# Kernel tuning notes

Hardware: AMD Instinct MI355X
Metric: run time of the kernel (lower is better)

Reference implementation:

```python
import jax, jax.numpy as jnp
import numpy as np

FEATURE_DIM = 512
HIDDEN_DIM = 512
N_HEADS = 8
HEAD_DIM = HIDDEN_DIM // N_HEADS
MAX_LEN = 5000
GAMMA = 0.5  # gaussian relative-position bias width
LN_EPS = 1e-5


def make_pe(d_model, max_len):
    # sinusoidal positional encoding buffer, as in PositionalEncoding.__init__
    pos = jnp.arange(max_len, dtype=jnp.float32)[:, None]
    div = jnp.exp(jnp.arange(0, d_model, 2, dtype=jnp.float32) * (-np.log(10000.0) / d_model))
    ang = pos * div  # [max_len, d_model/2]
    pe = jnp.zeros((max_len, d_model), dtype=jnp.float32)
    pe = pe.at[:, 0::2].set(jnp.sin(ang)).at[:, 1::2].set(jnp.cos(ang))
    return pe


def setup_inputs() -> dict:
    key = jax.random.key(0)
    k_x, k_q, k_k, k_v = jax.random.split(key, 4)
    xavier = np.sqrt(6.0 / (FEATURE_DIM + HEAD_DIM))  # xavier_uniform over last two dims
    return {
        "data_window": jax.random.normal(k_x, (1, 2048, FEATURE_DIM), dtype=jnp.float32),
        "W_query": jax.random.uniform(k_q, (N_HEADS, FEATURE_DIM, HEAD_DIM), jnp.float32, -xavier, xavier),
        "W_key": jax.random.uniform(k_k, (N_HEADS, FEATURE_DIM, HEAD_DIM), jnp.float32, -xavier, xavier),
        "W_value": jax.random.uniform(k_v, (N_HEADS, FEATURE_DIM, HEAD_DIM), jnp.float32, -xavier, xavier),
        "ln_gamma": jnp.ones((FEATURE_DIM,), dtype=jnp.float32),
        "ln_beta": jnp.zeros((FEATURE_DIM,), dtype=jnp.float32),
    }


def reference(data_window, W_query, W_key, W_value, ln_gamma, ln_beta):
    B, S, F = data_window.shape
    temperature = 1.0

    # LayerNorm over feature dim
    mu = jnp.mean(data_window, axis=-1, keepdims=True)
    var = jnp.mean(jnp.square(data_window - mu), axis=-1, keepdims=True)
    x = (data_window - mu) * jax.lax.rsqrt(var + LN_EPS) * ln_gamma + ln_beta

    # positional encoding, exactly as original: x + pe[:x.shape[0]] (requires B==1)
    pe = make_pe(FEATURE_DIM, MAX_LEN)
    x = x + pe[:B]  # [B,F] broadcasts over [B,S,F] only because B==1

    # per-head QKV projections, vectorized over heads
    Q = jnp.einsum('bsf,hfd->bhsd', x, W_query)
    K = jnp.einsum('bsf,hfd->bhsd', x, W_key)
    V = jnp.einsum('bsf,hfd->bhsd', x, W_value)

    scores = jnp.einsum('bhsd,bhtd->bhst', Q, K) / np.sqrt(HEAD_DIM)

    # gaussian relative-position bias: scale(=1) * exp(-gamma * (i-j)^2)
    p = jnp.arange(S, dtype=jnp.float32)
    rel = p[:, None] - p[None, :]
    bias = jnp.exp(-GAMMA * jnp.square(rel))  # [S,S]
    scores = (scores + bias[None, None]) / temperature
    # dropout on scores is identity in eval mode

    attn = jax.nn.softmax(scores, axis=-1)  # [B,H,S,S]
    head_out = jnp.einsum('bhst,bhtd->bhsd', attn, V)

    # concat heads along feature dim: [B,S,H*D]
    multi_head_output = head_out.transpose(0, 2, 1, 3).reshape(B, S, N_HEADS * HEAD_DIM)
    mean_weights = jnp.mean(attn, axis=1)  # [B,S,S]
    return multi_head_output, mean_weights
```

## Files before the change

kernel.cpp:

```cpp
#include <hip/hip_runtime.h>
#include <hip/hip_bf16.h>
#include <math.h>

#define S_LEN 2048
#define FDIM  512
#define NH    8
#define HD    64
#define MH_ELEMS (S_LEN * FDIM)
#define MEAN_ELEMS (S_LEN * S_LEN)

typedef _Float16 half_t;
typedef _Float16 half2v __attribute__((ext_vector_type(2)));
typedef _Float16 half4v __attribute__((ext_vector_type(4)));
typedef _Float16 half8v __attribute__((ext_vector_type(8)));
typedef float    float4v __attribute__((ext_vector_type(4)));
typedef int      int4v   __attribute__((ext_vector_type(4)));

#define MFMA16(a, b, c) __builtin_amdgcn_mfma_f32_16x16x32_f16((a), (b), (c), 0, 0, 0)

__global__ __launch_bounds__(256) void prep_kernel(const float* __restrict__ x,
                                                   const float* __restrict__ gamma,
                                                   const float* __restrict__ beta,
                                                   const float* __restrict__ Wq,
                                                   const float* __restrict__ Wk,
                                                   const float* __restrict__ Wv,
                                                   half_t* __restrict__ xo,
                                                   half_t* __restrict__ WT) {
    const int tid = threadIdx.x;
    if (blockIdx.x < 2048) {
        const int row = blockIdx.x;
        const float2 v = ((const float2*)(x + (size_t)row * FDIM))[tid];
        float s = v.x + v.y;
        float q = v.x * v.x + v.y * v.y;
        #pragma unroll
        for (int off = 1; off < 64; off <<= 1) {
            s += __shfl_xor(s, off, 64);
            q += __shfl_xor(q, off, 64);
        }
        __shared__ float red[8];
        const int wave = tid >> 6;
        if ((tid & 63) == 0) { red[wave] = s; red[4 + wave] = q; }
        __syncthreads();
        s = red[0] + red[1] + red[2] + red[3];
        q = red[4] + red[5] + red[6] + red[7];
        const float mu  = s * (1.0f / FDIM);
        const float var = q * (1.0f / FDIM) - mu * mu;
        const float rstd = rsqrtf(var + 1e-5f);
        const int f0 = tid * 2, f1 = tid * 2 + 1;
        const float o0 = (v.x - mu) * rstd * gamma[f0] + beta[f0];
        const float o1 = (v.y - mu) * rstd * gamma[f1] + beta[f1] + 1.0f;
        half2v o; o.x = (half_t)o0; o.y = (half_t)o1;
        ((half2v*)(xo + (size_t)row * FDIM))[tid] = o;
    } else {
        const int idx = blockIdx.x - 2048;
        const int k0 = (idx & 7) * 64;
        const int h  = (idx >> 3) & 7;
        const int z  = idx >> 6;
        const float* W = ((z == 0) ? Wq : (z == 1) ? Wk : Wv) + (size_t)h * FDIM * HD;
        __shared__ float Ls[64][65];
        {
            const int kk = tid >> 2, dg = (tid & 3) * 16;
            #pragma unroll
            for (int j = 0; j < 4; ++j) {
                const float4 w = *(const float4*)(W + (size_t)(k0 + kk) * HD + dg + j * 4);
                Ls[kk][dg + j * 4 + 0] = w.x; Ls[kk][dg + j * 4 + 1] = w.y;
                Ls[kk][dg + j * 4 + 2] = w.z; Ls[kk][dg + j * 4 + 3] = w.w;
            }
        }
        __syncthreads();
        {
            const int d = tid >> 2, kg = (tid & 3) * 16;
            half8v t0, t1;
            #pragma unroll
            for (int j = 0; j < 8; ++j) t0[j] = (half_t)Ls[kg + j][d];
            #pragma unroll
            for (int j = 0; j < 8; ++j) t1[j] = (half_t)Ls[kg + 8 + j][d];
            half_t* dst = WT + ((size_t)(z * NH + h) * HD + d) * FDIM + k0 + kg;
            *(half8v*)dst = t0;
            *(half8v*)(dst + 8) = t1;
        }
    }
}

__global__ __launch_bounds__(256) void qkv_kernel(const half_t* __restrict__ xh,
                                                  const half_t* __restrict__ WT,
                                                  half_t* __restrict__ Qo,
                                                  half_t* __restrict__ Ko,
                                                  half_t* __restrict__ VTo) {
    const int ms0 = blockIdx.x * 128;
    const int h   = blockIdx.y, z = blockIdx.z;
    const half_t* Wt = WT + (size_t)(z * NH + h) * HD * FDIM;

    const int tid = threadIdx.x;
    const int wv = tid >> 6, lane = tid & 63;
    const int lo = lane & 15, qq = lane >> 4;

    float4v acc[2][4];
    #pragma unroll
    for (int rg = 0; rg < 2; ++rg)
        #pragma unroll
        for (int cg = 0; cg < 4; ++cg) acc[rg][cg] = (float4v){0.f, 0.f, 0.f, 0.f};

    const half_t* ar[2];
    ar[0] = xh + (size_t)(ms0 + wv * 32 + lo) * FDIM + qq * 8;
    ar[1] = ar[0] + 16 * FDIM;
    const half_t* wrow[4];
    #pragma unroll
    for (int cg = 0; cg < 4; ++cg) wrow[cg] = Wt + (size_t)(cg * 16 + lo) * FDIM + qq * 8;

    half8v a_c[2][2], b_c[4][2];
    #pragma unroll
    for (int rg = 0; rg < 2; ++rg) { a_c[rg][0] = *(const half8v*)(ar[rg]); a_c[rg][1] = *(const half8v*)(ar[rg] + 32); }
    #pragma unroll
    for (int cg = 0; cg < 4; ++cg) { b_c[cg][0] = *(const half8v*)(wrow[cg]); b_c[cg][1] = *(const half8v*)(wrow[cg] + 32); }

    for (int k0 = 0; k0 < FDIM; k0 += 64) {
        const int kn0 = (k0 + 64 < FDIM) ? k0 + 64 : 0;
        const int kn1 = (k0 + 96 < FDIM) ? k0 + 96 : 0;
        half8v a_n[2][2], b_n[4][2];
        #pragma unroll
        for (int rg = 0; rg < 2; ++rg) { a_n[rg][0] = *(const half8v*)(ar[rg] + kn0); a_n[rg][1] = *(const half8v*)(ar[rg] + kn1); }
        #pragma unroll
        for (int cg = 0; cg < 4; ++cg) { b_n[cg][0] = *(const half8v*)(wrow[cg] + kn0); b_n[cg][1] = *(const half8v*)(wrow[cg] + kn1); }
        #pragma unroll
        for (int kh = 0; kh < 2; ++kh)
            #pragma unroll
            for (int rg = 0; rg < 2; ++rg)
                #pragma unroll
                for (int cg = 0; cg < 4; ++cg)
                    acc[rg][cg] = MFMA16(a_c[rg][kh], b_c[cg][kh], acc[rg][cg]);
        #pragma unroll
        for (int rg = 0; rg < 2; ++rg) { a_c[rg][0] = a_n[rg][0]; a_c[rg][1] = a_n[rg][1]; }
        #pragma unroll
        for (int cg = 0; cg < 4; ++cg) { b_c[cg][0] = b_n[cg][0]; b_c[cg][1] = b_n[cg][1]; }
    }

    if (z < 2) {
        half_t* Co = ((z == 0) ? Qo : Ko) + (size_t)h * S_LEN * HD;
        #pragma unroll
        for (int rg = 0; rg < 2; ++rg)
            #pragma unroll
            for (int cg = 0; cg < 4; ++cg)
                #pragma unroll
                for (int r = 0; r < 4; ++r)
                    Co[(size_t)(ms0 + wv * 32 + rg * 16 + qq * 4 + r) * HD + cg * 16 + lo] =
                        (half_t)acc[rg][cg][r];
    } else {
        __shared__ float Ls[128][65];
        #pragma unroll
        for (int rg = 0; rg < 2; ++rg)
            #pragma unroll
            for (int cg = 0; cg < 4; ++cg)
                #pragma unroll
                for (int r = 0; r < 4; ++r)
                    Ls[wv * 32 + rg * 16 + qq * 4 + r][cg * 16 + lo] = acc[rg][cg][r];
        __syncthreads();
        const int d = tid & 63, sg = tid >> 6;
        half_t* dst = VTo + (size_t)(h * HD + d) * S_LEN + ms0 + sg * 32;
        #pragma unroll
        for (int c = 0; c < 4; ++c) {
            half8v t;
            #pragma unroll
            for (int j = 0; j < 8; ++j) t[j] = (half_t)Ls[sg * 32 + c * 8 + j][d];
            *(half8v*)(dst + c * 8) = t;
        }
    }
}

__global__ __launch_bounds__(256) void attn2_kernel(const half_t* __restrict__ Qw,
                                                    const half_t* __restrict__ Kw,
                                                    const half_t* __restrict__ VT,
                                                    half_t* __restrict__ Op,
                                                    float* __restrict__ mp,
                                                    float* __restrict__ lp) {
    const int s0 = blockIdx.x * 32;
    const int h  = blockIdx.y;
    const int z  = blockIdx.z;
    const half_t* Qh = Qw + (size_t)h * S_LEN * HD;
    const half_t* Kh = Kw + (size_t)h * S_LEN * HD;
    const half_t* Vt = VT + (size_t)h * (size_t)HD * S_LEN;

    __shared__ float Osh[4][32][65];
    __shared__ float lsh[4][32];
    __shared__ float msh[4][32];

    const int tid = threadIdx.x;
    const int wv = tid >> 6, lane = tid & 63;
    const int lo = lane & 15, qq = lane >> 4;
    const int tb = z * 1024 + wv * 256;

    const half8v qA0 = *(const half8v*)(Qh + (size_t)(s0 + lo) * HD + qq * 8);
    const half8v qA1 = *(const half8v*)(Qh + (size_t)(s0 + lo) * HD + 32 + qq * 8);
    const half8v qB0 = *(const half8v*)(Qh + (size_t)(s0 + 16 + lo) * HD + qq * 8);
    const half8v qB1 = *(const half8v*)(Qh + (size_t)(s0 + 16 + lo) * HD + 32 + qq * 8);

    float4v accA[4], accB[4];
    #pragma unroll
    for (int dt = 0; dt < 4; ++dt) {
        accA[dt] = (float4v){0.f, 0.f, 0.f, 0.f};
        accB[dt] = (float4v){0.f, 0.f, 0.f, 0.f};
    }
    float mA = 0.f, mB = 0.f, lA = 0.f, lB = 0.f;

    const int srcLow  = lo + ((qq & 1) * 2) * 16;
    const int srcHigh = srcLow + 16;
    const bool sel1 = (qq >> 1) != 0;

    half8v kc[4];
    {
        const half_t* kp0 = Kh + (size_t)(tb + lo) * HD;
        const half_t* kp1 = Kh + (size_t)(tb + 16 + lo) * HD;
        kc[0] = *(const half8v*)(kp0 + qq * 8);
        kc[1] = *(const half8v*)(kp0 + 32 + qq * 8);
        kc[2] = *(const half8v*)(kp1 + qq * 8);
        kc[3] = *(const half8v*)(kp1 + 32 + qq * 8);
    }

    for (int ps = 0; ps < 8; ++ps) {
        const int Tg  = tb + ps * 32;
        const int Tgn = tb + ((ps < 7) ? ps + 1 : ps) * 32;
        half8v kn[4], vc[4];
        {
            const half_t* kp0 = Kh + (size_t)(Tgn + lo) * HD;
            const half_t* kp1 = Kh + (size_t)(Tgn + 16 + lo) * HD;
            kn[0] = *(const half8v*)(kp0 + qq * 8);
            kn[1] = *(const half8v*)(kp0 + 32 + qq * 8);
            kn[2] = *(const half8v*)(kp1 + qq * 8);
            kn[3] = *(const half8v*)(kp1 + 32 + qq * 8);
            #pragma unroll
            for (int dt = 0; dt < 4; ++dt)
                vc[dt] = *(const half8v*)(Vt + (size_t)(dt * 16 + lo) * S_LEN + Tg + qq * 8);
        }
        float4v c0A = (float4v){0.f, 0.f, 0.f, 0.f};
        c0A = MFMA16(kc[0], qA0, c0A); c0A = MFMA16(kc[1], qA1, c0A);
        float4v c1A = (float4v){0.f, 0.f, 0.f, 0.f};
        c1A = MFMA16(kc[2], qA0, c1A); c1A = MFMA16(kc[3], qA1, c1A);
        float4v c0B = (float4v){0.f, 0.f, 0.f, 0.f};
        c0B = MFMA16(kc[0], qB0, c0B); c0B = MFMA16(kc[1], qB1, c0B);
        float4v c1B = (float4v){0.f, 0.f, 0.f, 0.f};
        c1B = MFMA16(kc[2], qB0, c1B); c1B = MFMA16(kc[3], qB1, c1B);

        const int dd0 = s0 - Tg;
        const bool nA0 = (dd0 > -40) && (dd0 < 40);
        const bool nA1 = (dd0 - 16 > -40) && (dd0 - 16 < 40);
        const bool nB0 = (dd0 + 16 > -40) && (dd0 + 16 < 40);
        const bool nB1 = nA0;
        float S0A[4], S1A[4], S0B[4], S1B[4];
        #pragma unroll
        for (int r = 0; r < 4; ++r) {
            const int t0 = Tg + qq * 4 + r, t1 = t0 + 16;
            float sa0 = c0A[r] * 0.125f;
            if (nA0) { const float d = (float)(s0 + lo - t0); sa0 += __expf(-0.5f * d * d); }
            float sa1 = c1A[r] * 0.125f;
            if (nA1) { const float d = (float)(s0 + lo - t1); sa1 += __expf(-0.5f * d * d); }
            float sb0 = c0B[r] * 0.125f;
            if (nB0) { const float d = (float)(s0 + 16 + lo - t0); sb0 += __expf(-0.5f * d * d); }
            float sb1 = c1B[r] * 0.125f;
            if (nB1) { const float d = (float)(s0 + 16 + lo - t1); sb1 += __expf(-0.5f * d * d); }
            S0A[r] = sa0; S1A[r] = sa1; S0B[r] = sb0; S1B[r] = sb1;
        }
        float smA = fmaxf(fmaxf(fmaxf(S0A[0], S0A[1]), fmaxf(S0A[2], S0A[3])),
                          fmaxf(fmaxf(S1A[0], S1A[1]), fmaxf(S1A[2], S1A[3])));
        float smB = fmaxf(fmaxf(fmaxf(S0B[0], S0B[1]), fmaxf(S0B[2], S0B[3])),
                          fmaxf(fmaxf(S1B[0], S1B[1]), fmaxf(S1B[2], S1B[3])));
        smA = fmaxf(smA, __shfl_xor(smA, 16, 64));
        smA = fmaxf(smA, __shfl_xor(smA, 32, 64));
        smB = fmaxf(smB, __shfl_xor(smB, 16, 64));
        smB = fmaxf(smB, __shfl_xor(smB, 32, 64));
        const float mnA = fmaxf(mA, smA), mnB = fmaxf(mB, smB);
        const float alA = __expf(mA - mnA), alB = __expf(mB - mnB);
        mA = mnA; mB = mnB;
        float E0A[4], E1A[4], E0B[4], E1B[4];
        float lsA = 0.f, lsB = 0.f;
        #pragma unroll
        for (int r = 0; r < 4; ++r) {
            E0A[r] = __expf(S0A[r] - mnA); E1A[r] = __expf(S1A[r] - mnA);
            E0B[r] = __expf(S0B[r] - mnB); E1B[r] = __expf(S1B[r] - mnB);
            lsA += E0A[r] + E1A[r];
            lsB += E0B[r] + E1B[r];
        }
        lA = lA * alA + lsA;
        lB = lB * alB + lsB;
        #pragma unroll
        for (int dt = 0; dt < 4; ++dt)
            #pragma unroll
            for (int i = 0; i < 4; ++i) { accA[dt][i] *= alA; accB[dt][i] *= alB; }

        int pkA0, pkA1, pkA2, pkA3, pkB0, pkB1, pkB2, pkB3;
        {
            half2v p;
            p.x = (half_t)E0A[0]; p.y = (half_t)E0A[1]; pkA0 = __builtin_bit_cast(int, p);
            p.x = (half_t)E0A[2]; p.y = (half_t)E0A[3]; pkA1 = __builtin_bit_cast(int, p);
            p.x = (half_t)E1A[0]; p.y = (half_t)E1A[1]; pkA2 = __builtin_bit_cast(int, p);
            p.x = (half_t)E1A[2]; p.y = (half_t)E1A[3]; pkA3 = __builtin_bit_cast(int, p);
            p.x = (half_t)E0B[0]; p.y = (half_t)E0B[1]; pkB0 = __builtin_bit_cast(int, p);
            p.x = (half_t)E0B[2]; p.y = (half_t)E0B[3]; pkB1 = __builtin_bit_cast(int, p);
            p.x = (half_t)E1B[0]; p.y = (half_t)E1B[1]; pkB2 = __builtin_bit_cast(int, p);
            p.x = (half_t)E1B[2]; p.y = (half_t)E1B[3]; pkB3 = __builtin_bit_cast(int, p);
        }
        int4v biA, biB;
        {
            const int l0a = __shfl(pkA0, srcLow, 64),  l0b = __shfl(pkA2, srcLow, 64);
            const int l1a = __shfl(pkA1, srcLow, 64),  l1b = __shfl(pkA3, srcLow, 64);
            const int h0a = __shfl(pkA0, srcHigh, 64), h0b = __shfl(pkA2, srcHigh, 64);
            const int h1a = __shfl(pkA1, srcHigh, 64), h1b = __shfl(pkA3, srcHigh, 64);
            biA[0] = sel1 ? l0b : l0a;
            biA[1] = sel1 ? l1b : l1a;
            biA[2] = sel1 ? h0b : h0a;
            biA[3] = sel1 ? h1b : h1a;
        }
        {
            const int l0a = __shfl(pkB0, srcLow, 64),  l0b = __shfl(pkB2, srcLow, 64);
            const int l1a = __shfl(pkB1, srcLow, 64),  l1b = __shfl(pkB3, srcLow, 64);
            const int h0a = __shfl(pkB0, srcHigh, 64), h0b = __shfl(pkB2, srcHigh, 64);
            const int h1a = __shfl(pkB1, srcHigh, 64), h1b = __shfl(pkB3, srcHigh, 64);
            biB[0] = sel1 ? l0b : l0a;
            biB[1] = sel1 ? l1b : l1a;
            biB[2] = sel1 ? h0b : h0a;
            biB[3] = sel1 ? h1b : h1a;
        }
        const half8v bpA = __builtin_bit_cast(half8v, biA);
        const half8v bpB = __builtin_bit_cast(half8v, biB);
        #pragma unroll
        for (int dt = 0; dt < 4; ++dt) {
            accA[dt] = MFMA16(vc[dt], bpA, accA[dt]);
            accB[dt] = MFMA16(vc[dt], bpB, accB[dt]);
        }
        #pragma unroll
        for (int i = 0; i < 4; ++i) kc[i] = kn[i];
    }

    lA += __shfl_xor(lA, 16, 64); lA += __shfl_xor(lA, 32, 64);
    lB += __shfl_xor(lB, 16, 64); lB += __shfl_xor(lB, 32, 64);
    if (qq == 0) {
        lsh[wv][lo] = lA;      msh[wv][lo] = mA;
        lsh[wv][16 + lo] = lB; msh[wv][16 + lo] = mB;
    }
    #pragma unroll
    for (int dt = 0; dt < 4; ++dt)
        #pragma unroll
        for (int r = 0; r < 4; ++r) {
            Osh[wv][lo][dt * 16 + qq * 4 + r]      = accA[dt][r];
            Osh[wv][16 + lo][dt * 16 + qq * 4 + r] = accB[dt][r];
        }
    __syncthreads();

    #pragma unroll
    for (int p = 0; p < 2; ++p) {
        const int q = p * 16 + (tid >> 4), dg = tid & 15;
        const float m0 = msh[0][q], m1 = msh[1][q], m2 = msh[2][q], m3 = msh[3][q];
        const float M = fmaxf(fmaxf(m0, m1), fmaxf(m2, m3));
        const float f0 = __expf(m0 - M), f1 = __expf(m1 - M);
        const float f2 = __expf(m2 - M), f3 = __expf(m3 - M);
        const float L = lsh[0][q] * f0 + lsh[1][q] * f1 + lsh[2][q] * f2 + lsh[3][q] * f3;
        half4v o;
        #pragma unroll
        for (int i = 0; i < 4; ++i) {
            const float ov = Osh[0][q][dg * 4 + i] * f0 + Osh[1][q][dg * 4 + i] * f1 +
                             Osh[2][q][dg * 4 + i] * f2 + Osh[3][q][dg * 4 + i] * f3;
            o[i] = (half_t)ov;
        }
        const size_t pidx = (size_t)(z * NH + h) * S_LEN + s0 + q;
        *(half4v*)(Op + pidx * HD + dg * 4) = o;
        if (dg == 0) { mp[pidx] = M; lp[pidx] = L; }
    }
}

__global__ __launch_bounds__(256) void mean2_kernel(const half_t* __restrict__ Qw,
                                                    const half_t* __restrict__ Kw,
                                                    const half_t* __restrict__ Op,
                                                    const float* __restrict__ mp,
                                                    const float* __restrict__ lp,
                                                    float* __restrict__ out) {
    const int q0 = blockIdx.x * 32;
    const int tbase = blockIdx.y * 128;
    const int tid = threadIdx.x;

    __shared__ float lnc[NH][32];
    __shared__ float g0s[NH][32];
    __shared__ float g1s[NH][32];
    {
        const int h = tid >> 5, qi = tid & 31;
        const size_t i0 = (size_t)h * S_LEN + q0 + qi;
        const size_t i1 = (size_t)(NH + h) * S_LEN + q0 + qi;
        const float m0 = mp[i0], m1 = mp[i1];
        const float M = fmaxf(m0, m1);
        const float f0 = __expf(m0 - M), f1 = __expf(m1 - M);
        const float L = lp[i0] * f0 + lp[i1] * f1;
        const float inv = 1.0f / L;
        lnc[h][qi] = -M - __logf(L);
        g0s[h][qi] = f0 * inv;
        g1s[h][qi] = f1 * inv;
    }
    __syncthreads();

    const int wv = tid >> 6, lane = tid & 63;
    const int lo = lane & 15, qq = lane >> 4;
    const int t0 = tbase + wv * 32;

    float4v macc[2][2];
    #pragma unroll
    for (int rg = 0; rg < 2; ++rg)
        #pragma unroll
        for (int tg = 0; tg < 2; ++tg) macc[rg][tg] = (float4v){0.f, 0.f, 0.f, 0.f};

    const half_t* qp = Qw + (size_t)(q0 + lo) * HD + qq * 8;
    const half_t* kp = Kw + (size_t)(t0 + lo) * HD + qq * 8;

    #pragma unroll 2
    for (int h = 0; h < NH; ++h) {
        half8v a[2][2], b[2][2];
        #pragma unroll
        for (int rg = 0; rg < 2; ++rg) {
            a[rg][0] = *(const half8v*)(qp + (size_t)rg * 16 * HD);
            a[rg][1] = *(const half8v*)(qp + (size_t)rg * 16 * HD + 32);
        }
        #pragma unroll
        for (int tg = 0; tg < 2; ++tg) {
            b[tg][0] = *(const half8v*)(kp + (size_t)tg * 16 * HD);
            b[tg][1] = *(const half8v*)(kp + (size_t)tg * 16 * HD + 32);
        }
        float4v sacc[2][2];
        #pragma unroll
        for (int rg = 0; rg < 2; ++rg)
            #pragma unroll
            for (int tg = 0; tg < 2; ++tg) sacc[rg][tg] = (float4v){0.f, 0.f, 0.f, 0.f};
        #pragma unroll
        for (int kh = 0; kh < 2; ++kh)
            #pragma unroll
            for (int rg = 0; rg < 2; ++rg)
                #pragma unroll
                for (int tg = 0; tg < 2; ++tg)
                    sacc[rg][tg] = MFMA16(a[rg][kh], b[tg][kh], sacc[rg][tg]);

        const float4v ln0 = *(const float4v*)&lnc[h][qq * 4];
        const float4v ln1 = *(const float4v*)&lnc[h][16 + qq * 4];
        #pragma unroll
        for (int tg = 0; tg < 2; ++tg)
            #pragma unroll
            for (int r = 0; r < 4; ++r) {
                macc[0][tg][r] += __expf(fmaf(sacc[0][tg][r], 0.125f, ln0[r]));
                macc[1][tg][r] += __expf(fmaf(sacc[1][tg][r], 0.125f, ln1[r]));
            }
        qp += (size_t)S_LEN * HD;
        kp += (size_t)S_LEN * HD;
    }

    const bool near = ((q0 + 31 - t0) > -40) && ((q0 - (t0 + 31)) < 40);
    #pragma unroll
    for (int rg = 0; rg < 2; ++rg)
        #pragma unroll
        for (int tg = 0; tg < 2; ++tg)
            #pragma unroll
            for (int r = 0; r < 4; ++r) {
                const int qe = q0 + rg * 16 + qq * 4 + r;
                const int te = t0 + tg * 16 + lo;
                float w = macc[rg][tg][r] * 0.125f;
                if (near) {
                    const float d = (float)(qe - te);
                    w *= __expf(__expf(-0.5f * d * d));
                }
                out[MH_ELEMS + (size_t)qe * S_LEN + te] = w;
            }

    if (blockIdx.y == 0) {
        const int qi = tid >> 3, dg = (tid & 7) * 8;
        const int q = q0 + qi;
        #pragma unroll
        for (int h = 0; h < NH; ++h) {
            const half8v o0 = *(const half8v*)(Op + ((size_t)h * S_LEN + q) * HD + dg);
            const half8v o1 = *(const half8v*)(Op + ((size_t)(NH + h) * S_LEN + q) * HD + dg);
            const float a0 = g0s[h][qi], a1 = g1s[h][qi];
            float4 r0, r1;
            r0.x = (float)o0[0] * a0 + (float)o1[0] * a1;
            r0.y = (float)o0[1] * a0 + (float)o1[1] * a1;
            r0.z = (float)o0[2] * a0 + (float)o1[2] * a1;
            r0.w = (float)o0[3] * a0 + (float)o1[3] * a1;
            r1.x = (float)o0[4] * a0 + (float)o1[4] * a1;
            r1.y = (float)o0[5] * a0 + (float)o1[5] * a1;
            r1.z = (float)o0[6] * a0 + (float)o1[6] * a1;
            r1.w = (float)o0[7] * a0 + (float)o1[7] * a1;
            float* dst = out + (size_t)q * FDIM + h * HD + dg;
            *(float4*)dst = r0;
            *(float4*)(dst + 4) = r1;
        }
    }
}

extern "C" void kernel_launch(void* const* d_in, const int* in_sizes, int n_in,
                              void* d_out, int out_size, void* d_ws, size_t ws_size,
                              hipStream_t stream) {
    const float* x  = (const float*)d_in[0];
    const float* Wq = (const float*)d_in[1];
    const float* Wk = (const float*)d_in[2];
    const float* Wv = (const float*)d_in[3];
    const float* g  = (const float*)d_in[4];
    const float* b  = (const float*)d_in[5];
    float* out = (float*)d_out;
    char*  ws  = (char*)d_ws;

    half_t* Qh   = (half_t*)(ws);
    half_t* Kh   = (half_t*)(ws + (2ull  << 20));
    half_t* VT   = (half_t*)(ws + (4ull  << 20));
    half_t* xh   = (half_t*)(ws + (6ull  << 20));
    half_t* WT   = (half_t*)(ws + (8ull  << 20));
    half_t* Op   = (half_t*)(ws + (10ull << 20));
    float*  mp   = (float*) (ws + (14ull << 20));
    float*  lp   = (float*) (ws + (14ull << 20) + (128ull << 10));

    prep_kernel<<<2240, 256, 0, stream>>>(x, g, b, Wq, Wk, Wv, xh, WT);
    qkv_kernel<<<dim3(16, 8, 3), 256, 0, stream>>>(xh, WT, Qh, Kh, VT);
    attn2_kernel<<<dim3(64, 8, 2), 256, 0, stream>>>(Qh, Kh, VT, Op, mp, lp);
    mean2_kernel<<<dim3(64, 16), 256, 0, stream>>>(Qh, Kh, Op, mp, lp, out);
}
```

Measured before the change: 166.1 us.

## Use exp2 softmax with lazy rescaling and widen mean kernel key tile

The attention kernel now scales scores by log2(e) and uses the hardware exp2 instruction. It skips the running-max rescale of the accumulators unless some lane's max grows by more than a threshold, and stores the max in natural-log units for the later kernel. The mean-weights kernel now has each wave cover 64 keys instead of 32 and launches half as many blocks, which reuses the loaded Q fragments across more MFMAs. The costs are more registers per thread in the mean kernel and fewer blocks in flight, while lazy rescaling keeps exponentials bounded by the threshold.

```diff
diff --git a/kernel.cpp b/kernel.cpp
--- a/kernel.cpp
+++ b/kernel.cpp
@@ -8,6 +8,8 @@
 #define HD    64
 #define MH_ELEMS (S_LEN * FDIM)
 #define MEAN_ELEMS (S_LEN * S_LEN)
+#define LOG2E 1.44269504f
+#define LN2   0.69314718f
 
 typedef _Float16 half_t;
 typedef _Float16 half2v __attribute__((ext_vector_type(2)));
@@ -17,6 +19,10 @@
 typedef int      int4v   __attribute__((ext_vector_type(4)));
 
 #define MFMA16(a, b, c) __builtin_amdgcn_mfma_f32_16x16x32_f16((a), (b), (c), 0, 0, 0)
+
+static __device__ __forceinline__ float fast_exp2(float x) {
+    return __builtin_amdgcn_exp2f(x);
+}
 
 __global__ __launch_bounds__(256) void prep_kernel(const float* __restrict__ x,
                                                    const float* __restrict__ gamma,
@@ -257,7 +263,8 @@
             if (nB0) { const float d = (float)(s0 + 16 + lo - t0); sb0 += __expf(-0.5f * d * d); }
             float sb1 = c1B[r] * 0.125f;
             if (nB1) { const float d = (float)(s0 + 16 + lo - t1); sb1 += __expf(-0.5f * d * d); }
-            S0A[r] = sa0; S1A[r] = sa1; S0B[r] = sb0; S1B[r] = sb1;
+            S0A[r] = sa0 * LOG2E; S1A[r] = sa1 * LOG2E;
+            S0B[r] = sb0 * LOG2E; S1B[r] = sb1 * LOG2E;
         }
         float smA = fmaxf(fmaxf(fmaxf(S0A[0], S0A[1]), fmaxf(S0A[2], S0A[3])),
                           fmaxf(fmaxf(S1A[0], S1A[1]), fmaxf(S1A[2], S1A[3])));
@@ -267,24 +274,28 @@
         smA = fmaxf(smA, __shfl_xor(smA, 32, 64));
         smB = fmaxf(smB, __shfl_xor(smB, 16, 64));
         smB = fmaxf(smB, __shfl_xor(smB, 32, 64));
-        const float mnA = fmaxf(mA, smA), mnB = fmaxf(mB, smB);
-        const float alA = __expf(mA - mnA), alB = __expf(mB - mnB);
-        mA = mnA; mB = mnB;
+        const float gmax = fmaxf(smA - mA, smB - mB);
+        if (!__all(gmax <= 5.77f)) {
+            const float mnA = fmaxf(mA, smA), mnB = fmaxf(mB, smB);
+            const float alA = fast_exp2(mA - mnA), alB = fast_exp2(mB - mnB);
+            mA = mnA; mB = mnB;
+            lA *= alA; lB *= alB;
+            #pragma unroll
+            for (int dt = 0; dt < 4; ++dt)
+                #pragma unroll
+                for (int i = 0; i < 4; ++i) { accA[dt][i] *= alA; accB[dt][i] *= alB; }
+        }
         float E0A[4], E1A[4], E0B[4], E1B[4];
         float lsA = 0.f, lsB = 0.f;
         #pragma unroll
         for (int r = 0; r < 4; ++r) {
-            E0A[r] = __expf(S0A[r] - mnA); E1A[r] = __expf(S1A[r] - mnA);
-            E0B[r] = __expf(S0B[r] - mnB); E1B[r] = __expf(S1B[r] - mnB);
+            E0A[r] = fast_exp2(S0A[r] - mA); E1A[r] = fast_exp2(S1A[r] - mA);
+            E0B[r] = fast_exp2(S0B[r] - mB); E1B[r] = fast_exp2(S1B[r] - mB);
             lsA += E0A[r] + E1A[r];
             lsB += E0B[r] + E1B[r];
         }
-        lA = lA * alA + lsA;
-        lB = lB * alB + lsB;
-        #pragma unroll
-        for (int dt = 0; dt < 4; ++dt)
-            #pragma unroll
-            for (int i = 0; i < 4; ++i) { accA[dt][i] *= alA; accB[dt][i] *= alB; }
+        lA += lsA;
+        lB += lsB;
 
         int pkA0, pkA1, pkA2, pkA3, pkB0, pkB1, pkB2, pkB3;
         {
@@ -350,8 +361,8 @@
         const int q = p * 16 + (tid >> 4), dg = tid & 15;
         const float m0 = msh[0][q], m1 = msh[1][q], m2 = msh[2][q], m3 = msh[3][q];
         const float M = fmaxf(fmaxf(m0, m1), fmaxf(m2, m3));
-        const float f0 = __expf(m0 - M), f1 = __expf(m1 - M);
-        const float f2 = __expf(m2 - M), f3 = __expf(m3 - M);
+        const float f0 = fast_exp2(m0 - M), f1 = fast_exp2(m1 - M);
+        const float f2 = fast_exp2(m2 - M), f3 = fast_exp2(m3 - M);
         const float L = lsh[0][q] * f0 + lsh[1][q] * f1 + lsh[2][q] * f2 + lsh[3][q] * f3;
         half4v o;
         #pragma unroll
@@ -362,7 +373,7 @@
         }
         const size_t pidx = (size_t)(z * NH + h) * S_LEN + s0 + q;
         *(half4v*)(Op + pidx * HD + dg * 4) = o;
-        if (dg == 0) { mp[pidx] = M; lp[pidx] = L; }
+        if (dg == 0) { mp[pidx] = M * LN2; lp[pidx] = L; }
     }
 }
 
@@ -373,7 +384,7 @@
                                                     const float* __restrict__ lp,
                                                     float* __restrict__ out) {
     const int q0 = blockIdx.x * 32;
-    const int tbase = blockIdx.y * 128;
+    const int tbase = blockIdx.y * 256;
     const int tid = threadIdx.x;
 
     __shared__ float lnc[NH][32];
@@ -396,47 +407,47 @@
 
     const int wv = tid >> 6, lane = tid & 63;
     const int lo = lane & 15, qq = lane >> 4;
-    const int t0 = tbase + wv * 32;
-
-    float4v macc[2][2];
+    const int t0 = tbase + wv * 64;
+
+    float4v macc[2][4];
     #pragma unroll
     for (int rg = 0; rg < 2; ++rg)
         #pragma unroll
-        for (int tg = 0; tg < 2; ++tg) macc[rg][tg] = (float4v){0.f, 0.f, 0.f, 0.f};
+        for (int tg = 0; tg < 4; ++tg) macc[rg][tg] = (float4v){0.f, 0.f, 0.f, 0.f};
 
     const half_t* qp = Qw + (size_t)(q0 + lo) * HD + qq * 8;
     const half_t* kp = Kw + (size_t)(t0 + lo) * HD + qq * 8;
 
     #pragma unroll 2
     for (int h = 0; h < NH; ++h) {
-        half8v a[2][2], b[2][2];
+        half8v a[2][2], b[4][2];
         #pragma unroll
         for (int rg = 0; rg < 2; ++rg) {
             a[rg][0] = *(const half8v*)(qp + (size_t)rg * 16 * HD);
             a[rg][1] = *(const half8v*)(qp + (size_t)rg * 16 * HD + 32);
         }
         #pragma unroll
-        for (int tg = 0; tg < 2; ++tg) {
+        for (int tg = 0; tg < 4; ++tg) {
             b[tg][0] = *(const half8v*)(kp + (size_t)tg * 16 * HD);
             b[tg][1] = *(const half8v*)(kp + (size_t)tg * 16 * HD + 32);
         }
-        float4v sacc[2][2];
+        float4v sacc[2][4];
         #pragma unroll
         for (int rg = 0; rg < 2; ++rg)
             #pragma unroll
-            for (int tg = 0; tg < 2; ++tg) sacc[rg][tg] = (float4v){0.f, 0.f, 0.f, 0.f};
+            for (int tg = 0; tg < 4; ++tg) sacc[rg][tg] = (float4v){0.f, 0.f, 0.f, 0.f};
         #pragma unroll
         for (int kh = 0; kh < 2; ++kh)
             #pragma unroll
             for (int rg = 0; rg < 2; ++rg)
                 #pragma unroll
-                for (int tg = 0; tg < 2; ++tg)
+                for (int tg = 0; tg < 4; ++tg)
                     sacc[rg][tg] = MFMA16(a[rg][kh], b[tg][kh], sacc[rg][tg]);
 
         const float4v ln0 = *(const float4v*)&lnc[h][qq * 4];
         const float4v ln1 = *(const float4v*)&lnc[h][16 + qq * 4];
         #pragma unroll
-        for (int tg = 0; tg < 2; ++tg)
+        for (int tg = 0; tg < 4; ++tg)
             #pragma unroll
             for (int r = 0; r < 4; ++r) {
                 macc[0][tg][r] += __expf(fmaf(sacc[0][tg][r], 0.125f, ln0[r]));
@@ -446,15 +457,16 @@
         kp += (size_t)S_LEN * HD;
     }
 
-    const bool near = ((q0 + 31 - t0) > -40) && ((q0 - (t0 + 31)) < 40);
     #pragma unroll
     for (int rg = 0; rg < 2; ++rg)
         #pragma unroll
-        for (int tg = 0; tg < 2; ++tg)
+        for (int tg = 0; tg < 4; ++tg) {
+            const int tgl = t0 + tg * 16;
+            const bool near = ((q0 + 31 - tgl) > -40) && ((q0 - (tgl + 15)) < 40);
             #pragma unroll
             for (int r = 0; r < 4; ++r) {
                 const int qe = q0 + rg * 16 + qq * 4 + r;
-                const int te = t0 + tg * 16 + lo;
+                const int te = tgl + lo;
                 float w = macc[rg][tg][r] * 0.125f;
                 if (near) {
                     const float d = (float)(qe - te);
@@ -462,6 +474,7 @@
                 }
                 out[MH_ELEMS + (size_t)qe * S_LEN + te] = w;
             }
+        }
 
     if (blockIdx.y == 0) {
         const int qi = tid >> 3, dg = (tid & 7) * 8;
@@ -511,5 +524,5 @@
     prep_kernel<<<2240, 256, 0, stream>>>(x, g, b, Wq, Wk, Wv, xh, WT);
     qkv_kernel<<<dim3(16, 8, 3), 256, 0, stream>>>(xh, WT, Qh, Kh, VT);
     attn2_kernel<<<dim3(64, 8, 2), 256, 0, stream>>>(Qh, Kh, VT, Op, mp, lp);
-    mean2_kernel<<<dim3(64, 16), 256, 0, stream>>>(Qh, Kh, Op, mp, lp, out);
+    mean2_kernel<<<dim3(64, 8), 256, 0, stream>>>(Qh, Kh, Op, mp, lp, out);
 }
```

Measured after the change: 161.3 us. 1.03x faster.
